# Performance work log

Hardware: AMD Instinct MI355X
Metric: run time of the kernel (lower is better)

Reference implementation:

```python
import jax, jax.numpy as jnp
import numpy as np

B, S, D = 2, 2048, 1024
H, HD = 16, 64


def setup_inputs() -> dict:
    key = jax.random.key(0)
    ks = jax.random.split(key, 10)
    scale = 1.0 / np.sqrt(D)
    inputs_q = jax.random.normal(ks[0], (B, S, D), dtype=jnp.float32)
    inputs_kv = jax.random.normal(ks[1], (B, S, D), dtype=jnp.float32)
    # causal mask, broadcast over batch: True = attend
    mask = jnp.broadcast_to(jnp.tril(jnp.ones((S, S), dtype=bool)), (B, S, S))
    Wq = jax.random.normal(ks[2], (D, H * HD), dtype=jnp.float32) * scale
    bq = jnp.zeros((H * HD,), dtype=jnp.float32)
    Wk = jax.random.normal(ks[3], (D, H * HD), dtype=jnp.float32) * scale
    bk = jnp.zeros((H * HD,), dtype=jnp.float32)
    Wv = jax.random.normal(ks[4], (D, H * HD), dtype=jnp.float32) * scale
    bv = jnp.zeros((H * HD,), dtype=jnp.float32)
    Wo = jax.random.normal(ks[5], (H * HD, D), dtype=jnp.float32) * scale
    bo = jnp.zeros((D,), dtype=jnp.float32)
    return {"inputs_q": inputs_q, "inputs_kv": inputs_kv, "mask": mask,
            "Wq": Wq, "bq": bq, "Wk": Wk, "bk": bk, "Wv": Wv, "bv": bv,
            "Wo": Wo, "bo": bo}


def reference(inputs_q, inputs_kv, mask, Wq, bq, Wk, bk, Wv, bv, Wo, bo):
    b, s_q, _ = inputs_q.shape
    s_k = inputs_kv.shape[1]
    # projections -> [B, S, H, HD]
    q = (inputs_q @ Wq + bq).reshape(b, s_q, H, HD)
    k = (inputs_kv @ Wk + bk).reshape(b, s_k, H, HD)
    v = (inputs_kv @ Wv + bv).reshape(b, s_k, H, HD)
    q = q / jnp.sqrt(jnp.asarray(HD, dtype=q.dtype))
    # scores: [B, H, Sq, Sk]
    attn = jnp.einsum('bqhd,bkhd->bhqk', q, k)
    m = mask[:, None, :, :]  # [B,1,Sq,Sk] broadcast over heads
    attn = jnp.where(m, attn, jnp.asarray(-1e30, dtype=attn.dtype))
    attn = jax.nn.softmax(attn, axis=-1)
    # dropout_rate = 0.0, deterministic -> identity
    out = jnp.einsum('bhqk,bkhd->bqhd', attn, v).reshape(b, s_q, H * HD)
    return out @ Wo + bo
```

## Files before the change

kernel.cpp:

```cpp
#include <hip/hip_runtime.h>

typedef __attribute__((ext_vector_type(4))) float f32x4;
typedef __attribute__((ext_vector_type(8))) short bf16x8;
typedef unsigned short u16;
typedef unsigned int u32;

#define AS1 __attribute__((address_space(1)))
#define AS3 __attribute__((address_space(3)))

__device__ __forceinline__ float fast_exp2(float x){
  return __builtin_amdgcn_exp2f(x);
}

__device__ __forceinline__ u16 f2bf(float x){
  u32 u = __float_as_uint(x);
  u += 0x7fffu + ((u >> 16) & 1u);
  return (u16)(u >> 16);
}
__device__ __forceinline__ u16 f2bf_fast(float x){
  return (u16)((__float_as_uint(x) + 0x8000u) >> 16);
}

__global__ __launch_bounds__(256) void cvt_qkv(const float* __restrict__ s0,
                                               const float* __restrict__ s1,
                                               u16* __restrict__ d0,
                                               u16* __restrict__ d1, int n4)
{
  int i = blockIdx.x * 256 + threadIdx.x;
  if (i >= n4) return;
  const float* src = blockIdx.y ? s1 : s0;
  u16* dst = blockIdx.y ? d1 : d0;
  float4 v = reinterpret_cast<const float4*>(src)[i];
  ushort4 o;
  o.x = f2bf(v.x); o.y = f2bf(v.y); o.z = f2bf(v.z); o.w = f2bf(v.w);
  reinterpret_cast<ushort4*>(dst)[i] = o;
}

__global__ __launch_bounds__(256) void transpose_cvt4(const float* __restrict__ W0,
                                                      const float* __restrict__ W1,
                                                      const float* __restrict__ W2,
                                                      const float* __restrict__ W3,
                                                      u16* __restrict__ dst)
{
  __shared__ float tile[32][33];
  const int z = blockIdx.z;
  const float* src = z == 0 ? W0 : z == 1 ? W1 : z == 2 ? W2 : W3;
  u16* d = dst + (size_t)z * 1024 * 1024;
  int tx = threadIdx.x & 31, ty = threadIdx.x >> 5;
  int k0 = blockIdx.x * 32, n0 = blockIdx.y * 32;
  for (int r = 0; r < 4; ++r)
    tile[ty + r * 8][tx] = src[(size_t)(k0 + ty + r * 8) * 1024 + n0 + tx];
  __syncthreads();
  for (int r = 0; r < 4; ++r)
    d[(size_t)(n0 + ty + r * 8) * 1024 + k0 + tx] = f2bf(tile[tx][ty + r * 8]);
}

__global__ __launch_bounds__(256) void transpose_bf16_b(const u16* __restrict__ src,
                                                        u16* __restrict__ dst, int R, int C)
{
  __shared__ u16 tile[32][34];
  int bb = blockIdx.z;
  const u16* s = src + (size_t)bb * R * C;
  u16* d = dst + (size_t)bb * C * R;
  int r0 = blockIdx.x * 32, c0 = blockIdx.y * 32;
  int tx = threadIdx.x & 31, ty = threadIdx.x >> 5;
  for (int r = 0; r < 4; ++r)
    tile[ty + r * 8][tx] = s[(size_t)(r0 + ty + r * 8) * C + c0 + tx];
  __syncthreads();
  for (int r = 0; r < 4; ++r)
    d[(size_t)(c0 + ty + r * 8) * R + r0 + tx] = tile[tx][ty + r * 8];
}

__global__ __launch_bounds__(256) void gemm_qkv(const u16* __restrict__ Xq,
                                                const u16* __restrict__ Xkv,
                                                const u16* __restrict__ Wt,
                                                const float* __restrict__ bq,
                                                const float* __restrict__ bk,
                                                const float* __restrict__ bv,
                                                u16* __restrict__ Qb,
                                                u16* __restrict__ Kb,
                                                u16* __restrict__ Vb,
                                                int M, int K)
{
  __shared__ u16 lA[128 * 32];
  __shared__ u16 lB[128 * 32];
  const int tid = threadIdx.x;
  const int l = tid & 63, w = tid >> 6;
  const int wr = w >> 1, wc = w & 1;
  const int bm0 = blockIdx.x * 128, bn0 = blockIdx.y * 128;
  const int seg = bn0 >> 10;
  const int nloc0 = bn0 & 1023;
  const u16* A = seg ? Xkv : Xq;
  const float* bias = seg == 0 ? bq : seg == 1 ? bk : bv;
  u16* C = seg == 0 ? Qb : seg == 1 ? Kb : Vb;
  const float scale = seg == 0 ? 0.125f * 1.44269504089f : 1.0f;
  const int lr = l & 15, lg = (l >> 4) * 8;

  f32x4 acc[4][4];
#pragma unroll
  for (int m = 0; m < 4; ++m)
#pragma unroll
    for (int n = 0; n < 4; ++n) acc[m][n] = (f32x4){0.f, 0.f, 0.f, 0.f};

  for (int k0 = 0; k0 < K; k0 += 32){
#pragma unroll
    for (int c = 0; c < 2; ++c){
      int e = (c * 256 + tid) * 8;
      int row = e >> 5, col = e & 31;
      __builtin_amdgcn_global_load_lds(
          (const AS1 u32*)(A + (size_t)(bm0 + row) * K + k0 + col),
          (AS3 u32*)(&lA[e]), 16, 0, 0);
      __builtin_amdgcn_global_load_lds(
          (const AS1 u32*)(Wt + (size_t)(bn0 + row) * K + k0 + col),
          (AS3 u32*)(&lB[e]), 16, 0, 0);
    }
    __syncthreads();
    bf16x8 aF[4], bF[4];
#pragma unroll
    for (int m = 0; m < 4; ++m)
      aF[m] = *reinterpret_cast<const bf16x8*>(&lA[(wr * 64 + m * 16 + lr) * 32 + lg]);
#pragma unroll
    for (int n = 0; n < 4; ++n)
      bF[n] = *reinterpret_cast<const bf16x8*>(&lB[(wc * 64 + n * 16 + lr) * 32 + lg]);
    __builtin_amdgcn_s_setprio(1);
#pragma unroll
    for (int m = 0; m < 4; ++m)
#pragma unroll
      for (int n = 0; n < 4; ++n)
        acc[m][n] = __builtin_amdgcn_mfma_f32_16x16x32_bf16(aF[m], bF[n], acc[m][n], 0, 0, 0);
    __builtin_amdgcn_s_setprio(0);
    __syncthreads();
  }

  const int r0 = (l >> 4) * 4;
#pragma unroll
  for (int m = 0; m < 4; ++m){
#pragma unroll
    for (int n = 0; n < 4; ++n){
      int col = nloc0 + wc * 64 + n * 16 + lr;
      float bv_ = bias[col];
#pragma unroll
      for (int r = 0; r < 4; ++r){
        int row = bm0 + wr * 64 + m * 16 + r0 + r;
        C[(size_t)row * 1024 + col] = f2bf((acc[m][n][r] + bv_) * scale);
      }
    }
  }
}

__global__ __launch_bounds__(256) void gemm_out(const u16* __restrict__ A,
                                                const u16* __restrict__ Bt,
                                                const float* __restrict__ bias,
                                                float* __restrict__ Cf,
                                                int M, int N, int K)
{
  __shared__ u16 lA[64 * 32];
  __shared__ u16 lB[128 * 32];
  const int tid = threadIdx.x;
  const int l = tid & 63, w = tid >> 6;
  const int wr = w >> 1, wc = w & 1;
  const int bm0 = blockIdx.x * 64, bn0 = blockIdx.y * 128;
  const int lr = l & 15, lg = (l >> 4) * 8;

  f32x4 acc[2][4];
#pragma unroll
  for (int m = 0; m < 2; ++m)
#pragma unroll
    for (int n = 0; n < 4; ++n) acc[m][n] = (f32x4){0.f, 0.f, 0.f, 0.f};

  for (int k0 = 0; k0 < K; k0 += 32){
    {
      int e = tid * 8;
      int row = e >> 5, col = e & 31;
      __builtin_amdgcn_global_load_lds(
          (const AS1 u32*)(A + (size_t)(bm0 + row) * K + k0 + col),
          (AS3 u32*)(&lA[e]), 16, 0, 0);
    }
#pragma unroll
    for (int c = 0; c < 2; ++c){
      int e = (c * 256 + tid) * 8;
      int row = e >> 5, col = e & 31;
      __builtin_amdgcn_global_load_lds(
          (const AS1 u32*)(Bt + (size_t)(bn0 + row) * K + k0 + col),
          (AS3 u32*)(&lB[e]), 16, 0, 0);
    }
    __syncthreads();
    bf16x8 aF[2], bF[4];
#pragma unroll
    for (int m = 0; m < 2; ++m)
      aF[m] = *reinterpret_cast<const bf16x8*>(&lA[(wr * 32 + m * 16 + lr) * 32 + lg]);
#pragma unroll
    for (int n = 0; n < 4; ++n)
      bF[n] = *reinterpret_cast<const bf16x8*>(&lB[(wc * 64 + n * 16 + lr) * 32 + lg]);
    __builtin_amdgcn_s_setprio(1);
#pragma unroll
    for (int m = 0; m < 2; ++m)
#pragma unroll
      for (int n = 0; n < 4; ++n)
        acc[m][n] = __builtin_amdgcn_mfma_f32_16x16x32_bf16(aF[m], bF[n], acc[m][n], 0, 0, 0);
    __builtin_amdgcn_s_setprio(0);
    __syncthreads();
  }

  const int r0 = (l >> 4) * 4;
#pragma unroll
  for (int m = 0; m < 2; ++m)
#pragma unroll
    for (int n = 0; n < 4; ++n){
      int col = bn0 + wc * 64 + n * 16 + lr;
      float bv_ = bias[col];
#pragma unroll
      for (int r = 0; r < 4; ++r){
        int row = bm0 + wr * 32 + m * 16 + r0 + r;
        Cf[(size_t)row * N + col] = acc[m][n][r] + bv_;
      }
    }
}


#define LOADK(KF, T) do{                                                      \
  const int kv0_ = (T) * 64;                                                  \
  _Pragma("unroll") for (int kc_ = 0; kc_ < 2; ++kc_)                         \
  _Pragma("unroll") for (int n_ = 0; n_ < 4; ++n_)                            \
    KF[kc_][n_] = *reinterpret_cast<const bf16x8*>(                           \
        Kb + baseQK + (size_t)(kv0_ + n_ * 16 + lr) * 1024 + kc_ * 32 + lg);  \
}while(0)

#define LOADV(VF, T) do{                                                      \
  const int kv0_ = (T) * 64;                                                  \
  _Pragma("unroll") for (int kc_ = 0; kc_ < 2; ++kc_)                         \
  _Pragma("unroll") for (int n_ = 0; n_ < 4; ++n_)                            \
    VF[kc_][n_] = *reinterpret_cast<const bf16x8*>(                           \
        Vt + baseVt + (size_t)(n_ * 16 + lr) * S + kv0_ + kc_ * 32 + lg);     \
}while(0)

#define ATTN_BODY(KF, VF, T) do{                                              \
  const int kv0_ = (T) * 64;                                                  \
  f32x4 sA_[2][4];                                                            \
  _Pragma("unroll") for (int m_ = 0; m_ < 2; ++m_)                            \
  _Pragma("unroll") for (int n_ = 0; n_ < 4; ++n_)                            \
    sA_[m_][n_] = (f32x4){0.f, 0.f, 0.f, 0.f};                                \
  __builtin_amdgcn_s_setprio(1);                                              \
  _Pragma("unroll") for (int m_ = 0; m_ < 2; ++m_)                            \
  _Pragma("unroll") for (int kc_ = 0; kc_ < 2; ++kc_)                         \
  _Pragma("unroll") for (int n_ = 0; n_ < 4; ++n_)                            \
    sA_[m_][n_] = __builtin_amdgcn_mfma_f32_16x16x32_bf16(                    \
        qf[m_][kc_], KF[kc_][n_], sA_[m_][n_], 0, 0, 0);                      \
  __builtin_amdgcn_s_setprio(0);                                              \
  if ((T) == ntw - 1){                                                        \
    _Pragma("unroll") for (int m_ = 0; m_ < 2; ++m_)                          \
    _Pragma("unroll") for (int n_ = 0; n_ < 4; ++n_){                         \
      int kvg_ = kv0_ + n_ * 16 + lr;                                         \
      _Pragma("unroll") for (int r_ = 0; r_ < 4; ++r_){                       \
        int qg_ = q0 + m_ * 16 + g4 * 4 + r_;                                 \
        float e_ = fast_exp2(sA_[m_][n_][r_]);                                \
        sA_[m_][n_][r_] = (kvg_ <= qg_) ? e_ : 0.f;                           \
      }                                                                       \
    }                                                                         \
  } else {                                                                    \
    _Pragma("unroll") for (int m_ = 0; m_ < 2; ++m_)                          \
    _Pragma("unroll") for (int n_ = 0; n_ < 4; ++n_)                          \
    _Pragma("unroll") for (int r_ = 0; r_ < 4; ++r_)                          \
      sA_[m_][n_][r_] = fast_exp2(sA_[m_][n_][r_]);                           \
  }                                                                           \
  _Pragma("unroll") for (int m_ = 0; m_ < 2; ++m_)                            \
  _Pragma("unroll") for (int n_ = 0; n_ < 4; ++n_)                            \
  _Pragma("unroll") for (int r_ = 0; r_ < 4; ++r_){                           \
    int row_ = m_ * 16 + g4 * 4 + r_;                                         \
    myP[row_ * 72 + n_ * 16 + lr] = f2bf_fast(sA_[m_][n_][r_]);               \
  }                                                                           \
  bf16x8 pf_[2][2];                                                           \
  _Pragma("unroll") for (int m_ = 0; m_ < 2; ++m_)                            \
  _Pragma("unroll") for (int kc_ = 0; kc_ < 2; ++kc_)                         \
    pf_[m_][kc_] = *reinterpret_cast<const bf16x8*>(                          \
        &myP[(m_ * 16 + lr) * 72 + (kc_ * 4 + g4) * 8]);                      \
  __builtin_amdgcn_s_setprio(1);                                              \
  _Pragma("unroll") for (int m_ = 0; m_ < 2; ++m_)                            \
  _Pragma("unroll") for (int kc_ = 0; kc_ < 2; ++kc_){                        \
    acc_l[m_] = __builtin_amdgcn_mfma_f32_16x16x32_bf16(                      \
        pf_[m_][kc_], ones, acc_l[m_], 0, 0, 0);                              \
    _Pragma("unroll") for (int n_ = 0; n_ < 4; ++n_)                          \
      acc_o[m_][n_] = __builtin_amdgcn_mfma_f32_16x16x32_bf16(                \
          pf_[m_][kc_], VF[kc_][n_], acc_o[m_][n_], 0, 0, 0);                 \
  }                                                                           \
  __builtin_amdgcn_s_setprio(0);                                              \
}while(0)

__global__ __launch_bounds__(256, 2) void attn_fwd(const u16* __restrict__ Qb,
                                                   const u16* __restrict__ Kb,
                                                   const u16* __restrict__ Vt,
                                                   u16* __restrict__ AO, int S)
{
  __shared__ u16 lP[4][32 * 72];
  const int tid = threadIdx.x, l = tid & 63, w = tid >> 6;
  const int j = blockIdx.x;
  const int bh = j & 31;
  const int qt = (j < 256) ? (j >> 5) : (15 - ((j >> 5) & 7));
  const int bb = bh >> 4;
  const size_t baseQK = ((size_t)bb * S) * 1024 + (bh & 15) * 64;
  const size_t baseVt = (size_t)bh * 64 * S;
  const int lr = l & 15, g4 = l >> 4, lg = g4 * 8;
  const int q0 = qt * 128 + w * 32;
  const int ntw = ((q0 + 31) >> 6) + 1;

  bf16x8 qf[2][2];
#pragma unroll
  for (int m = 0; m < 2; ++m)
#pragma unroll
    for (int kc = 0; kc < 2; ++kc)
      qf[m][kc] = *reinterpret_cast<const bf16x8*>(
          Qb + baseQK + (size_t)(q0 + m * 16 + lr) * 1024 + kc * 32 + lg);

  bf16x8 ones;
#pragma unroll
  for (int i = 0; i < 8; ++i) ones[i] = (short)0x3F80;

  f32x4 acc_o[2][4];
  f32x4 acc_l[2];
#pragma unroll
  for (int m = 0; m < 2; ++m){
    acc_l[m] = (f32x4){0.f, 0.f, 0.f, 0.f};
#pragma unroll
    for (int n = 0; n < 4; ++n) acc_o[m][n] = (f32x4){0.f, 0.f, 0.f, 0.f};
  }

  u16* myP = (u16*)lP[w];

  bf16x8 kfA[2][4], kfB[2][4];
  LOADK(kfA, 0);
  int t = 0;
  while (true){
    {
      bf16x8 vf_[2][4];
      LOADV(vf_, t);
      if (t + 1 < ntw) LOADK(kfB, t + 1);
      ATTN_BODY(kfA, vf_, t);
    }
    ++t; if (t == ntw) break;
    {
      bf16x8 vf_[2][4];
      LOADV(vf_, t);
      if (t + 1 < ntw) LOADK(kfA, t + 1);
      ATTN_BODY(kfB, vf_, t);
    }
    ++t; if (t == ntw) break;
  }

#pragma unroll
  for (int m = 0; m < 2; ++m){
    float inv[4];
#pragma unroll
    for (int r = 0; r < 4; ++r) inv[r] = 1.0f / acc_l[m][r];
#pragma unroll
    for (int n = 0; n < 4; ++n)
#pragma unroll
      for (int r = 0; r < 4; ++r){
        int row = q0 + m * 16 + g4 * 4 + r;
        AO[baseQK + (size_t)row * 1024 + n * 16 + lr] = f2bf(acc_o[m][n][r] * inv[r]);
      }
  }
}

extern "C" void kernel_launch(void* const* d_in, const int* in_sizes, int n_in,
                              void* d_out, int out_size, void* d_ws, size_t ws_size,
                              hipStream_t stream)
{
  const float* inq  = (const float*)d_in[0];
  const float* inkv = (const float*)d_in[1];
  const float* Wq = (const float*)d_in[3];
  const float* bq = (const float*)d_in[4];
  const float* Wk = (const float*)d_in[5];
  const float* bk = (const float*)d_in[6];
  const float* Wv = (const float*)d_in[7];
  const float* bv = (const float*)d_in[8];
  const float* Wo = (const float*)d_in[9];
  const float* bo = (const float*)d_in[10];
  float* out = (float*)d_out;

  const int B = 2, S = 2048, D = 1024;
  const int M = B * S;

  char* ws = (char*)d_ws;
  const size_t MB = 1024ull * 1024ull;
  u16* Xq  = (u16*)(ws + 0 * MB);
  u16* Vtg = (u16*)(ws + 0 * MB);
  u16* Xkv = (u16*)(ws + 8 * MB);
  u16* Wt  = (u16*)(ws + 16 * MB);
  u16* Wot = (u16*)(ws + 22 * MB);
  u16* Qb  = (u16*)(ws + 24 * MB);
  u16* Kb  = (u16*)(ws + 32 * MB);
  u16* Vb  = (u16*)(ws + 40 * MB);
  u16* AOb = (u16*)(ws + 48 * MB);

  cvt_qkv<<<dim3(M * D / 4 / 256, 2), 256, 0, stream>>>(inq, inkv, Xq, Xkv, M * D / 4);

  transpose_cvt4<<<dim3(32, 32, 4), 256, 0, stream>>>(Wq, Wk, Wv, Wo, Wt);

  gemm_qkv<<<dim3(M / 128, 3072 / 128), 256, 0, stream>>>(Xq, Xkv, Wt, bq, bk, bv,
                                                          Qb, Kb, Vb, M, D);

  transpose_bf16_b<<<dim3(S / 32, D / 32, B), 256, 0, stream>>>(Vb, Vtg, S, D);

  attn_fwd<<<dim3(512), 256, 0, stream>>>(Qb, Kb, Vtg, AOb, S);

  gemm_out<<<dim3(M / 64, D / 128), 256, 0, stream>>>(AOb, Wot, bo, out, M, D, D);
}
```

Before: 142.0 us.

## Pair low and high query rows per wave to balance causal attention work

Each wave now handles one 16-row query strip from the front and its mirror strip from the back of the sequence, so every wave does a near-constant number of KV tiles under the causal mask. This replaces contiguous 32-row strips, where waves near the diagonal start idled while late waves did most of the work. Block-to-head mapping is also changed so blocks for the same heads land on the same XCD, which should help K/V cache reuse. The cost is a conditional second half-body per tile and divergent loop lengths between the two strips. K/V loads are shared between them.

```diff
diff --git a/kernel.cpp b/kernel.cpp
--- a/kernel.cpp
+++ b/kernel.cpp
@@ -234,56 +234,57 @@
         Vt + baseVt + (size_t)(n_ * 16 + lr) * S + kv0_ + kc_ * 32 + lg);     \
 }while(0)
 
-#define ATTN_BODY(KF, VF, T) do{                                              \
+#define HALF_BODY(MI, KF, VF, T, Q0M, NTM) do{                                \
   const int kv0_ = (T) * 64;                                                  \
-  f32x4 sA_[2][4];                                                            \
-  _Pragma("unroll") for (int m_ = 0; m_ < 2; ++m_)                            \
+  f32x4 sA_[4];                                                               \
   _Pragma("unroll") for (int n_ = 0; n_ < 4; ++n_)                            \
-    sA_[m_][n_] = (f32x4){0.f, 0.f, 0.f, 0.f};                                \
+    sA_[n_] = (f32x4){0.f, 0.f, 0.f, 0.f};                                    \
   __builtin_amdgcn_s_setprio(1);                                              \
-  _Pragma("unroll") for (int m_ = 0; m_ < 2; ++m_)                            \
   _Pragma("unroll") for (int kc_ = 0; kc_ < 2; ++kc_)                         \
   _Pragma("unroll") for (int n_ = 0; n_ < 4; ++n_)                            \
-    sA_[m_][n_] = __builtin_amdgcn_mfma_f32_16x16x32_bf16(                    \
-        qf[m_][kc_], KF[kc_][n_], sA_[m_][n_], 0, 0, 0);                      \
+    sA_[n_] = __builtin_amdgcn_mfma_f32_16x16x32_bf16(                        \
+        qf[MI][kc_], KF[kc_][n_], sA_[n_], 0, 0, 0);                          \
   __builtin_amdgcn_s_setprio(0);                                              \
-  if ((T) == ntw - 1){                                                        \
-    _Pragma("unroll") for (int m_ = 0; m_ < 2; ++m_)                          \
+  if ((T) == (NTM) - 1){                                                      \
     _Pragma("unroll") for (int n_ = 0; n_ < 4; ++n_){                         \
       int kvg_ = kv0_ + n_ * 16 + lr;                                         \
       _Pragma("unroll") for (int r_ = 0; r_ < 4; ++r_){                       \
-        int qg_ = q0 + m_ * 16 + g4 * 4 + r_;                                 \
-        float e_ = fast_exp2(sA_[m_][n_][r_]);                                \
-        sA_[m_][n_][r_] = (kvg_ <= qg_) ? e_ : 0.f;                           \
+        int qg_ = (Q0M) + g4 * 4 + r_;                                        \
+        float e_ = fast_exp2(sA_[n_][r_]);                                    \
+        sA_[n_][r_] = (kvg_ <= qg_) ? e_ : 0.f;                               \
       }                                                                       \
     }                                                                         \
   } else {                                                                    \
-    _Pragma("unroll") for (int m_ = 0; m_ < 2; ++m_)                          \
     _Pragma("unroll") for (int n_ = 0; n_ < 4; ++n_)                          \
     _Pragma("unroll") for (int r_ = 0; r_ < 4; ++r_)                          \
-      sA_[m_][n_][r_] = fast_exp2(sA_[m_][n_][r_]);                           \
+      sA_[n_][r_] = fast_exp2(sA_[n_][r_]);                                   \
   }                                                                           \
-  _Pragma("unroll") for (int m_ = 0; m_ < 2; ++m_)                            \
   _Pragma("unroll") for (int n_ = 0; n_ < 4; ++n_)                            \
   _Pragma("unroll") for (int r_ = 0; r_ < 4; ++r_){                           \
-    int row_ = m_ * 16 + g4 * 4 + r_;                                         \
-    myP[row_ * 72 + n_ * 16 + lr] = f2bf_fast(sA_[m_][n_][r_]);               \
+    int row_ = (MI) * 16 + g4 * 4 + r_;                                       \
+    myP[row_ * 72 + n_ * 16 + lr] = f2bf_fast(sA_[n_][r_]);                   \
   }                                                                           \
-  bf16x8 pf_[2][2];                                                           \
-  _Pragma("unroll") for (int m_ = 0; m_ < 2; ++m_)                            \
+  bf16x8 pf_[2];                                                              \
   _Pragma("unroll") for (int kc_ = 0; kc_ < 2; ++kc_)                         \
-    pf_[m_][kc_] = *reinterpret_cast<const bf16x8*>(                          \
-        &myP[(m_ * 16 + lr) * 72 + (kc_ * 4 + g4) * 8]);                      \
+    pf_[kc_] = *reinterpret_cast<const bf16x8*>(                              \
+        &myP[((MI) * 16 + lr) * 72 + (kc_ * 4 + g4) * 8]);                    \
   __builtin_amdgcn_s_setprio(1);                                              \
-  _Pragma("unroll") for (int m_ = 0; m_ < 2; ++m_)                            \
   _Pragma("unroll") for (int kc_ = 0; kc_ < 2; ++kc_){                        \
-    acc_l[m_] = __builtin_amdgcn_mfma_f32_16x16x32_bf16(                      \
-        pf_[m_][kc_], ones, acc_l[m_], 0, 0, 0);                              \
+    acc_l[MI] = __builtin_amdgcn_mfma_f32_16x16x32_bf16(                      \
+        pf_[kc_], ones, acc_l[MI], 0, 0, 0);                                  \
     _Pragma("unroll") for (int n_ = 0; n_ < 4; ++n_)                          \
-      acc_o[m_][n_] = __builtin_amdgcn_mfma_f32_16x16x32_bf16(                \
-          pf_[m_][kc_], VF[kc_][n_], acc_o[m_][n_], 0, 0, 0);                 \
+      acc_o[MI][n_] = __builtin_amdgcn_mfma_f32_16x16x32_bf16(                \
+          pf_[kc_], VF[kc_][n_], acc_o[MI][n_], 0, 0, 0);                     \
   }                                                                           \
   __builtin_amdgcn_s_setprio(0);                                              \
+}while(0)
+
+#define ATTN_TILE(KF, T) do{                                                  \
+  bf16x8 vf_[2][4];                                                           \
+  LOADV(vf_, T);                                                              \
+  if ((T) + 1 < nt_hi) LOADK((((T) & 1) ? kfA : kfB), (T) + 1);               \
+  HALF_BODY(1, KF, vf_, T, q0_hi, nt_hi);                                     \
+  if ((T) < nt_lo) HALF_BODY(0, KF, vf_, T, q0_lo, nt_lo);                    \
 }while(0)
 
 __global__ __launch_bounds__(256, 2) void attn_fwd(const u16* __restrict__ Qb,
@@ -294,22 +295,29 @@
   __shared__ u16 lP[4][32 * 72];
   const int tid = threadIdx.x, l = tid & 63, w = tid >> 6;
   const int j = blockIdx.x;
-  const int bh = j & 31;
-  const int qt = (j < 256) ? (j >> 5) : (15 - ((j >> 5) & 7));
+  const int xcd = j & 7;
+  const int bh = xcd * 4 + ((j >> 3) & 3);
+  const int pr = j >> 5;
   const int bb = bh >> 4;
   const size_t baseQK = ((size_t)bb * S) * 1024 + (bh & 15) * 64;
   const size_t baseVt = (size_t)bh * 64 * S;
   const int lr = l & 15, g4 = l >> 4, lg = g4 * 8;
-  const int q0 = qt * 128 + w * 32;
-  const int ntw = ((q0 + 31) >> 6) + 1;
+
+  const int pc = pr * 4 + w;
+  const int a = pc >> 2;
+  const int nt_lo = a + 1;
+  const int nt_hi = 32 - a;
+  const int q0_lo = pc * 16;
+  const int q0_hi = (127 - pc) * 16;
 
   bf16x8 qf[2][2];
 #pragma unroll
-  for (int m = 0; m < 2; ++m)
-#pragma unroll
-    for (int kc = 0; kc < 2; ++kc)
-      qf[m][kc] = *reinterpret_cast<const bf16x8*>(
-          Qb + baseQK + (size_t)(q0 + m * 16 + lr) * 1024 + kc * 32 + lg);
+  for (int kc = 0; kc < 2; ++kc){
+    qf[0][kc] = *reinterpret_cast<const bf16x8*>(
+        Qb + baseQK + (size_t)(q0_lo + lr) * 1024 + kc * 32 + lg);
+    qf[1][kc] = *reinterpret_cast<const bf16x8*>(
+        Qb + baseQK + (size_t)(q0_hi + lr) * 1024 + kc * 32 + lg);
+  }
 
   bf16x8 ones;
 #pragma unroll
@@ -330,24 +338,15 @@
   LOADK(kfA, 0);
   int t = 0;
   while (true){
-    {
-      bf16x8 vf_[2][4];
-      LOADV(vf_, t);
-      if (t + 1 < ntw) LOADK(kfB, t + 1);
-      ATTN_BODY(kfA, vf_, t);
-    }
-    ++t; if (t == ntw) break;
-    {
-      bf16x8 vf_[2][4];
-      LOADV(vf_, t);
-      if (t + 1 < ntw) LOADK(kfA, t + 1);
-      ATTN_BODY(kfB, vf_, t);
-    }
-    ++t; if (t == ntw) break;
+    ATTN_TILE(kfA, t);
+    ++t; if (t == nt_hi) break;
+    ATTN_TILE(kfB, t);
+    ++t; if (t == nt_hi) break;
   }
 
 #pragma unroll
   for (int m = 0; m < 2; ++m){
+    const int q0m = m ? q0_hi : q0_lo;
     float inv[4];
 #pragma unroll
     for (int r = 0; r < 4; ++r) inv[r] = 1.0f / acc_l[m][r];
@@ -355,7 +354,7 @@
     for (int n = 0; n < 4; ++n)
 #pragma unroll
       for (int r = 0; r < 4; ++r){
-        int row = q0 + m * 16 + g4 * 4 + r;
+        int row = q0m + g4 * 4 + r;
         AO[baseQK + (size_t)row * 1024 + n * 16 + lr] = f2bf(acc_o[m][n][r] * inv[r]);
       }
   }
```

New measurement: 180.5 us. 1.27x slower.
